# Kernel optimization log

Hardware: AMD Instinct MI355X
Metric: run time of the kernel (lower is better)

## Reference

```python
import jax, jax.numpy as jnp
import numpy as np

N_HEADS = 8

def setup_inputs() -> dict:
    key = jax.random.key(0)
    ks = jax.random.split(key, 5)
    d = 256
    B, N = 2, 4096
    scale = 1.0 / np.sqrt(d)
    return {
        "x_q": jax.random.normal(ks[0], (B, N, d), jnp.float32),
        "x_kv": jax.random.normal(ks[1], (B, N, d), jnp.float32),
        "Wq": jax.random.normal(ks[2], (d, d), jnp.float32) * scale,
        "bq": jnp.zeros((d,), jnp.float32),
        "Wk": jax.random.normal(ks[3], (d, d), jnp.float32) * scale,
        "bk": jnp.zeros((d,), jnp.float32),
        "Wv": jax.random.normal(ks[4], (d, d), jnp.float32) * scale,
        "bv": jnp.zeros((d,), jnp.float32),
    }


def reference(x_q, x_kv, Wq, bq, Wk, bk, Wv, bv):
    B, Nq, d = x_q.shape
    H = N_HEADS
    dh = d // H
    # linear projections (torch Linear: x @ W^T + b)
    q = x_q @ Wq.T + bq            # [B, Nq, d]
    k = x_kv @ Wk.T + bk           # [B, Nk, d]
    v = x_kv @ Wv.T + bv           # [B, Nk, d]
    # split heads -> [B, H, N, dh]
    q = q.reshape(B, Nq, H, dh).transpose(0, 2, 1, 3)
    k = k.reshape(B, -1, H, dh).transpose(0, 2, 1, 3)
    v = v.reshape(B, -1, H, dh).transpose(0, 2, 1, 3)
    # scores [B, H, Nq, Nk], softmax over keys
    scores = jnp.einsum('bhqd,bhkd->bhqk', q, k) / jnp.sqrt(jnp.asarray(dh, q.dtype))
    attn = jax.nn.softmax(scores, axis=-1)
    out = jnp.einsum('bhqk,bhkd->bhqd', attn, v)   # [B, H, Nq, dh]
    return out.transpose(0, 2, 1, 3).reshape(B, Nq, H * dh)
```

## Files before the change

kernel.cpp:

```cpp
#include <hip/hip_runtime.h>
#include <stdint.h>

#define BATCH 2
#define NSEQ 4096
#define DM 256
#define NHEAD 8
#define DH 32
#define SCALE 0.17677669529663687f
#define QPRE (SCALE * 1.44269504088896340736f)

#if __has_builtin(__builtin_amdgcn_exp2f)
#define EXP2W(x) __builtin_amdgcn_exp2f(x)
#else
#define EXP2W(x) exp2f(x)
#endif

typedef unsigned short ushort_t;
typedef __attribute__((ext_vector_type(8))) short short8;
typedef __attribute__((ext_vector_type(4))) float float4v;

__device__ __forceinline__ ushort_t f2bf(float f) {
    union { float f; uint32_t i; } x; x.f = f;
    uint32_t i = x.i;
    i += ((i >> 16) & 1u) + 0x7fffu;
    return (ushort_t)(i >> 16);
}
__device__ __forceinline__ uint32_t rne16(float f) {
    const uint32_t i = __float_as_uint(f);
    return i + 0x7fffu + ((i >> 16) & 1u);
}
#if __has_builtin(__builtin_amdgcn_cvt_pk_bf16_f32)
typedef __bf16 bf16x2_t __attribute__((ext_vector_type(2)));
__device__ __forceinline__ uint32_t pk2(float a, float b) {
    union { bf16x2_t v; uint32_t u; } c;
    c.v = __builtin_amdgcn_cvt_pk_bf16_f32(a, b);
    return c.u;
}
#else
__device__ __forceinline__ uint32_t pk2(float a, float b) {
    return __builtin_amdgcn_perm(rne16(b), rne16(a), 0x07060302u);
}
#endif

__device__ __forceinline__ void load_lds_16B(const void* g, void* lds) {
    __builtin_amdgcn_global_load_lds(
        (const __attribute__((address_space(1))) void*)g,
        (__attribute__((address_space(3))) void*)lds, 16, 0, 0);
}

__global__ __launch_bounds__(256) void packw_kernel(
    const float* __restrict__ Wq, const float* __restrict__ Wk,
    const float* __restrict__ Wv, ushort_t* __restrict__ Wp)
{
    const int mat = blockIdx.x >> 5;
    const int off = (((blockIdx.x & 31) << 8) + threadIdx.x) * 8;
    const float* W = (mat == 0) ? Wq : (mat == 1) ? Wk : Wv;
    const float s  = (mat == 0) ? QPRE : 1.0f;
    float4 a = *(const float4*)(W + off);
    float4 b = *(const float4*)(W + off + 4);
    uint32_t d[4] = { pk2(a.x * s, a.y * s), pk2(a.z * s, a.w * s),
                      pk2(b.x * s, b.y * s), pk2(b.z * s, b.w * s) };
    *(uint4*)(Wp + (size_t)mat * (DM * DM) + off) = *(const uint4*)d;
}

#define RST 264
__global__ __launch_bounds__(256) void proj_kernel(
    const float* __restrict__ x_q, const float* __restrict__ x_kv,
    const ushort_t* __restrict__ Wp,
    const float* __restrict__ bq, const float* __restrict__ bk,
    const float* __restrict__ bv,
    ushort_t* __restrict__ Qh, ushort_t* __restrict__ Kh,
    ushort_t* __restrict__ Vt)
{
    const int mat = blockIdx.y;
    const int n0  = blockIdx.x * 32;
    const float* x    = (mat == 0) ? x_q : x_kv;
    const ushort_t* W = Wp + (size_t)mat * (DM * DM);
    const float* bias = (mat == 0) ? bq : (mat == 1) ? bk : bv;
    const float bscale = (mat == 0) ? QPRE : 1.0f;

    __shared__ __align__(16) ushort_t xls[32 * RST];
    const int t = threadIdx.x;
    {
        const int r  = t >> 3;
        const int c0 = (t & 7) * 32;
        const float* src = x + (size_t)(n0 + r) * DM + c0;
        uint32_t d[16];
        #pragma unroll
        for (int i = 0; i < 8; i++) {
            float4 v = *(const float4*)(src + i * 4);
            d[i * 2]     = pk2(v.x, v.y);
            d[i * 2 + 1] = pk2(v.z, v.w);
        }
        uint32_t* dst = (uint32_t*)&xls[r * RST + c0];
        #pragma unroll
        for (int i = 0; i < 4; i++)
            *(uint4*)(dst + i * 4) = *(const uint4*)&d[i * 4];
    }
    __syncthreads();

    const int w    = t >> 6;
    const int l    = t & 63;
    const int lm   = l & 15;
    const int quad = l >> 4;
    const int j0   = w * 64;

    float4v acc[2][4];
    #pragma unroll
    for (int rt = 0; rt < 2; rt++)
        #pragma unroll
        for (int jt = 0; jt < 4; jt++)
            acc[rt][jt] = (float4v){0.f, 0.f, 0.f, 0.f};

    for (int kc = 0; kc < DM / 32; kc++) {
        short8 af[2];
        #pragma unroll
        for (int rt = 0; rt < 2; rt++)
            af[rt] = *(const short8*)&xls[(rt * 16 + lm) * RST + kc * 32 + quad * 8];
        #pragma unroll
        for (int jt = 0; jt < 4; jt++) {
            short8 bf = *(const short8*)(W + (size_t)(j0 + jt * 16 + lm) * DM
                                           + kc * 32 + quad * 8);
            if (mat == 2) {
                acc[0][jt] = __builtin_amdgcn_mfma_f32_16x16x32_bf16(af[0], bf, acc[0][jt], 0, 0, 0);
                acc[1][jt] = __builtin_amdgcn_mfma_f32_16x16x32_bf16(af[1], bf, acc[1][jt], 0, 0, 0);
            } else {
                acc[0][jt] = __builtin_amdgcn_mfma_f32_16x16x32_bf16(bf, af[0], acc[0][jt], 0, 0, 0);
                acc[1][jt] = __builtin_amdgcn_mfma_f32_16x16x32_bf16(bf, af[1], acc[1][jt], 0, 0, 0);
            }
        }
    }

    const int bb = n0 >> 12;
    const int cn = n0 & (NSEQ - 1);
    if (mat == 2) {
        #pragma unroll
        for (int jt = 0; jt < 4; jt++) {
            const int j  = j0 + jt * 16 + lm;
            const int h  = j >> 5, dd = j & 31;
            const int bh = bb * NHEAD + h;
            const float bj = bias[j];
            #pragma unroll
            for (int rt = 0; rt < 2; rt++) {
                union { ushort_t u[4]; uint2 v; } pk;
                #pragma unroll
                for (int r = 0; r < 4; r++) pk.u[r] = f2bf(acc[rt][jt][r] + bj);
                *(uint2*)&Vt[((size_t)bh * DH + dd) * NSEQ + cn + quad * 8 + rt * 4] = pk.v;
            }
        }
    } else {
        ushort_t* dst = (mat == 0) ? Qh : Kh;
        #pragma unroll
        for (int jt = 0; jt < 4; jt++) {
            const int jb = j0 + jt * 16 + quad * 4;
            const int h  = jb >> 5, dd0 = jb & 31;
            const int bh = bb * NHEAD + h;
            float4 b4 = *(const float4*)(bias + jb);
            #pragma unroll
            for (int rt = 0; rt < 2; rt++) {
                const int n = cn + rt * 16 + lm;
                union { ushort_t u[4]; uint2 v; } pk;
                pk.u[0] = f2bf(acc[rt][jt][0] + b4.x * bscale);
                pk.u[1] = f2bf(acc[rt][jt][1] + b4.y * bscale);
                pk.u[2] = f2bf(acc[rt][jt][2] + b4.z * bscale);
                pk.u[3] = f2bf(acc[rt][jt][3] + b4.w * bscale);
                *(uint2*)&dst[((size_t)bh * NSEQ + n) * DH + dd0] = pk.v;
            }
        }
    }
}

#define QT 2
__global__ __launch_bounds__(256) void fattn_kernel(
    const ushort_t* __restrict__ Qh, const ushort_t* __restrict__ Kh,
    const ushort_t* __restrict__ Vt, float* __restrict__ out)
{
    const int blk  = blockIdx.x;
    const int xcd  = blk & 7;
    const int jj   = blk >> 3;
    const int bh   = xcd * 2 + (jj & 1);
    const int qblk = jj >> 1;
    const int b    = bh >> 3, h = bh & 7;

    const int w    = threadIdx.x >> 6;
    const int l    = threadIdx.x & 63;
    const int lm   = l & 15;
    const int quad = l >> 4;
    const int q0   = qblk * 128 + w * 32;

    __shared__ __align__(16) ushort_t tiles[2][2048];

    const ushort_t* Qb = Qh + (size_t)bh * NSEQ * DH;
    const ushort_t* Kb = Kh + (size_t)bh * NSEQ * DH;
    const ushort_t* Vb = Vt + (size_t)bh * DH * NSEQ;

    const ushort_t* gsrc;
    int gadv;
    if (w < 2) { gsrc = Kb + (size_t)(w * 16 + (l >> 2)) * DH + (l & 3) * 8;  gadv = 32 * DH; }
    else       { gsrc = Vb + (size_t)((w - 2) * 16 + (l >> 2)) * NSEQ + (l & 3) * 8; gadv = 32; }

    short8 qf[QT];
    #pragma unroll
    for (int qt = 0; qt < QT; qt++)
        qf[qt] = *(const short8*)(Qb + (size_t)(q0 + qt * 16 + lm) * DH + quad * 8);

    short8 ones;
    #pragma unroll
    for (int i = 0; i < 8; i++) ones[i] = (short)0x3F80;

    float4v accO[QT][2], accL[QT];
    #pragma unroll
    for (int qt = 0; qt < QT; qt++) {
        accO[qt][0] = (float4v){0.f, 0.f, 0.f, 0.f};
        accO[qt][1] = (float4v){0.f, 0.f, 0.f, 0.f};
        accL[qt]    = (float4v){0.f, 0.f, 0.f, 0.f};
    }
    const float4v zero = {0.f, 0.f, 0.f, 0.f};

    load_lds_16B(gsrc, &tiles[0][w * 512]);
    gsrc += gadv;

    for (int it = 0; it < NSEQ / 32; it++) {
        __syncthreads();
        if (it < NSEQ / 32 - 1) {
            load_lds_16B(gsrc, &tiles[(it + 1) & 1][w * 512]);
            gsrc += gadv;
        }

        const ushort_t* Kt = &tiles[it & 1][0];
        const ushort_t* Vl = &tiles[it & 1][1024];
        short8 kf0 = *(const short8*)&Kt[lm * 32 + quad * 8];
        short8 kf1 = *(const short8*)&Kt[512 + lm * 32 + quad * 8];
        short8 vf0 = *(const short8*)&Vl[lm * 32 + quad * 8];
        short8 vf1 = *(const short8*)&Vl[512 + lm * 32 + quad * 8];

        #pragma unroll
        for (int qt = 0; qt < QT; qt++) {
            float4v s0 = __builtin_amdgcn_mfma_f32_16x16x32_bf16(kf0, qf[qt], zero, 0, 0, 0);
            float4v s1 = __builtin_amdgcn_mfma_f32_16x16x32_bf16(kf1, qf[qt], zero, 0, 0, 0);
            float p0[4], p1[4];
            #pragma unroll
            for (int r = 0; r < 4; r++) {
                p0[r] = EXP2W(s0[r]);
                p1[r] = EXP2W(s1[r]);
            }
            uint32_t pd[4] = { pk2(p0[0], p0[1]), pk2(p0[2], p0[3]),
                               pk2(p1[0], p1[1]), pk2(p1[2], p1[3]) };
            short8 pf = *(const short8*)pd;
            accO[qt][0] = __builtin_amdgcn_mfma_f32_16x16x32_bf16(pf, vf0, accO[qt][0], 0, 0, 0);
            accO[qt][1] = __builtin_amdgcn_mfma_f32_16x16x32_bf16(pf, vf1, accO[qt][1], 0, 0, 0);
            accL[qt]    = __builtin_amdgcn_mfma_f32_16x16x32_bf16(pf, ones, accL[qt], 0, 0, 0);
        }
    }

    #pragma unroll
    for (int qt = 0; qt < QT; qt++)
        #pragma unroll
        for (int r = 0; r < 4; r++) {
            const float inv = 1.0f / accL[qt][r];
            const int q = q0 + qt * 16 + quad * 4 + r;
            float* orow = out + ((size_t)b * NSEQ + q) * DM + h * DH;
            orow[lm]      = accO[qt][0][r] * inv;
            orow[16 + lm] = accO[qt][1][r] * inv;
        }
}

extern "C" void kernel_launch(void* const* d_in, const int* in_sizes, int n_in,
                              void* d_out, int out_size, void* d_ws, size_t ws_size,
                              hipStream_t stream)
{
    const float* x_q  = (const float*)d_in[0];
    const float* x_kv = (const float*)d_in[1];
    const float* Wq   = (const float*)d_in[2];
    const float* bq   = (const float*)d_in[3];
    const float* Wk   = (const float*)d_in[4];
    const float* bk   = (const float*)d_in[5];
    const float* Wv   = (const float*)d_in[6];
    const float* bv   = (const float*)d_in[7];
    float* out = (float*)d_out;

    const size_t per = (size_t)BATCH * NHEAD * NSEQ * DH;
    ushort_t* Qh = (ushort_t*)d_ws;
    ushort_t* Kh = Qh + per;
    ushort_t* Vt = Kh + per;
    ushort_t* Wp = (ushort_t*)d_out;

    packw_kernel<<<96, 256, 0, stream>>>(Wq, Wk, Wv, Wp);

    dim3 pgrid(BATCH * NSEQ / 32, 3);
    proj_kernel<<<pgrid, 256, 0, stream>>>(x_q, x_kv, Wp, bq, bk, bv,
                                           Qh, Kh, Vt);

    fattn_kernel<<<512, 256, 0, stream>>>(Qh, Kh, Vt, out);
}
```

Measured before the change: 168.4 us.

## Split attention over key halves with a combine kernel for more blocks

Adds a split-K flash attention kernel: each of 1024 blocks handles half the keys and writes an unnormalized partial output and row sum, and a combine kernel adds the two halves and normalizes. This doubles the block count, so the 256 CUs of the GPU are better occupied than with 512 blocks. The cost is an extra launch and an extra read and write pass over the output-sized buffers. It also adds an explicit vmcnt(0) wait before the barrier in the tile loop of both kernels. That makes the async LDS loads visible, but it may serialize the prefetch.

Measured after the change: 168.5 us. No clear change (+0.0%).

```diff
diff --git a/kernel.cpp b/kernel.cpp
--- a/kernel.cpp
+++ b/kernel.cpp
@@ -14,6 +14,8 @@
 #else
 #define EXP2W(x) exp2f(x)
 #endif
+
+#define WAIT_VM0() asm volatile("s_waitcnt vmcnt(0)" ::: "memory")
 
 typedef unsigned short ushort_t;
 typedef __attribute__((ext_vector_type(8))) short short8;
@@ -221,6 +223,7 @@
     gsrc += gadv;
 
     for (int it = 0; it < NSEQ / 32; it++) {
+        WAIT_VM0();
         __syncthreads();
         if (it < NSEQ / 32 - 1) {
             load_lds_16B(gsrc, &tiles[(it + 1) & 1][w * 512]);
@@ -265,6 +268,133 @@
         }
 }
 
+#define KITERS 64
+__global__ __launch_bounds__(256) void fattn_split_kernel(
+    const ushort_t* __restrict__ Qh, const ushort_t* __restrict__ Kh,
+    const ushort_t* __restrict__ Vt, float* __restrict__ out,
+    float* __restrict__ Opart, float* __restrict__ Lp)
+{
+    const int blk  = blockIdx.x;
+    const int xcd  = blk & 7;
+    const int jj   = blk >> 3;
+    const int bh   = xcd * 2 + (jj & 1);
+    const int qblk = (jj >> 1) & 31;
+    const int khalf = jj >> 6;
+    const int b    = bh >> 3, h = bh & 7;
+
+    const int w    = threadIdx.x >> 6;
+    const int l    = threadIdx.x & 63;
+    const int lm   = l & 15;
+    const int quad = l >> 4;
+    const int q0   = qblk * 128 + w * 32;
+
+    __shared__ __align__(16) ushort_t tiles[2][2048];
+
+    const ushort_t* Qb = Qh + (size_t)bh * NSEQ * DH;
+    const ushort_t* Kb = Kh + (size_t)bh * NSEQ * DH + (size_t)khalf * 2048 * DH;
+    const ushort_t* Vb = Vt + (size_t)bh * DH * NSEQ + (size_t)khalf * 2048;
+
+    const ushort_t* gsrc;
+    int gadv;
+    if (w < 2) { gsrc = Kb + (size_t)(w * 16 + (l >> 2)) * DH + (l & 3) * 8;  gadv = 32 * DH; }
+    else       { gsrc = Vb + (size_t)((w - 2) * 16 + (l >> 2)) * NSEQ + (l & 3) * 8; gadv = 32; }
+
+    short8 qf[QT];
+    #pragma unroll
+    for (int qt = 0; qt < QT; qt++)
+        qf[qt] = *(const short8*)(Qb + (size_t)(q0 + qt * 16 + lm) * DH + quad * 8);
+
+    short8 ones;
+    #pragma unroll
+    for (int i = 0; i < 8; i++) ones[i] = (short)0x3F80;
+
+    float4v accO[QT][2], accL[QT];
+    #pragma unroll
+    for (int qt = 0; qt < QT; qt++) {
+        accO[qt][0] = (float4v){0.f, 0.f, 0.f, 0.f};
+        accO[qt][1] = (float4v){0.f, 0.f, 0.f, 0.f};
+        accL[qt]    = (float4v){0.f, 0.f, 0.f, 0.f};
+    }
+    const float4v zero = {0.f, 0.f, 0.f, 0.f};
+
+    load_lds_16B(gsrc, &tiles[0][w * 512]);
+    gsrc += gadv;
+
+    for (int it = 0; it < KITERS; it++) {
+        WAIT_VM0();
+        __syncthreads();
+        if (it < KITERS - 1) {
+            load_lds_16B(gsrc, &tiles[(it + 1) & 1][w * 512]);
+            gsrc += gadv;
+        }
+
+        const ushort_t* Kt = &tiles[it & 1][0];
+        const ushort_t* Vl = &tiles[it & 1][1024];
+        short8 kf0 = *(const short8*)&Kt[lm * 32 + quad * 8];
+        short8 kf1 = *(const short8*)&Kt[512 + lm * 32 + quad * 8];
+        short8 vf0 = *(const short8*)&Vl[lm * 32 + quad * 8];
+        short8 vf1 = *(const short8*)&Vl[512 + lm * 32 + quad * 8];
+
+        #pragma unroll
+        for (int qt = 0; qt < QT; qt++) {
+            float4v s0 = __builtin_amdgcn_mfma_f32_16x16x32_bf16(kf0, qf[qt], zero, 0, 0, 0);
+            float4v s1 = __builtin_amdgcn_mfma_f32_16x16x32_bf16(kf1, qf[qt], zero, 0, 0, 0);
+            float p0[4], p1[4];
+            #pragma unroll
+            for (int r = 0; r < 4; r++) {
+                p0[r] = EXP2W(s0[r]);
+                p1[r] = EXP2W(s1[r]);
+            }
+            uint32_t pd[4] = { pk2(p0[0], p0[1]), pk2(p0[2], p0[3]),
+                               pk2(p1[0], p1[1]), pk2(p1[2], p1[3]) };
+            short8 pf = *(const short8*)pd;
+            accO[qt][0] = __builtin_amdgcn_mfma_f32_16x16x32_bf16(pf, vf0, accO[qt][0], 0, 0, 0);
+            accO[qt][1] = __builtin_amdgcn_mfma_f32_16x16x32_bf16(pf, vf1, accO[qt][1], 0, 0, 0);
+            accL[qt]    = __builtin_amdgcn_mfma_f32_16x16x32_bf16(pf, ones, accL[qt], 0, 0, 0);
+        }
+    }
+
+    float* Od = (khalf == 0) ? out : Opart;
+    #pragma unroll
+    for (int qt = 0; qt < QT; qt++)
+        #pragma unroll
+        for (int r = 0; r < 4; r++) {
+            const int q = q0 + qt * 16 + quad * 4 + r;
+            float* orow = Od + ((size_t)b * NSEQ + q) * DM + h * DH;
+            orow[lm]      = accO[qt][0][r];
+            orow[16 + lm] = accO[qt][1][r];
+            if (lm == 0)
+                Lp[khalf * (16 * NSEQ) + bh * NSEQ + q] = accL[qt][r];
+        }
+}
+
+__global__ __launch_bounds__(256) void combine_kernel(
+    float* __restrict__ out, const float* __restrict__ Opart,
+    const float* __restrict__ Lp)
+{
+    const int t   = blockIdx.x * 256 + threadIdx.x;
+    const size_t base = (size_t)t * 8;
+    const int b   = (int)(base >> 20);
+    const int rem = (int)(base & ((1u << 20) - 1));
+    const int q   = rem >> 8;
+    const int dm  = rem & 255;
+    const int h   = dm >> 5;
+    const int bh  = b * NHEAD + h;
+    const float l0 = Lp[bh * NSEQ + q];
+    const float l1 = Lp[16 * NSEQ + bh * NSEQ + q];
+    const float inv = 1.0f / (l0 + l1);
+    float4 a0 = *(const float4*)(out + base);
+    float4 a1 = *(const float4*)(out + base + 4);
+    float4 c0 = *(const float4*)(Opart + base);
+    float4 c1 = *(const float4*)(Opart + base + 4);
+    a0.x = (a0.x + c0.x) * inv;  a0.y = (a0.y + c0.y) * inv;
+    a0.z = (a0.z + c0.z) * inv;  a0.w = (a0.w + c0.w) * inv;
+    a1.x = (a1.x + c1.x) * inv;  a1.y = (a1.y + c1.y) * inv;
+    a1.z = (a1.z + c1.z) * inv;  a1.w = (a1.w + c1.w) * inv;
+    *(float4*)(out + base)     = a0;
+    *(float4*)(out + base + 4) = a1;
+}
+
 extern "C" void kernel_launch(void* const* d_in, const int* in_sizes, int n_in,
                               void* d_out, int out_size, void* d_ws, size_t ws_size,
                               hipStream_t stream)
@@ -285,11 +415,23 @@
     ushort_t* Vt = Kh + per;
     ushort_t* Wp = (ushort_t*)d_out;
 
+    const size_t qkv_bytes   = per * 3 * sizeof(ushort_t);
+    const size_t opart_elems = (size_t)BATCH * NSEQ * DM;
+    const size_t lp_elems    = (size_t)2 * 16 * NSEQ;
+    const size_t need = qkv_bytes + (opart_elems + lp_elems) * sizeof(float);
+    float* Opart = (float*)((char*)d_ws + qkv_bytes);
+    float* Lp    = Opart + opart_elems;
+
     packw_kernel<<<96, 256, 0, stream>>>(Wq, Wk, Wv, Wp);
 
     dim3 pgrid(BATCH * NSEQ / 32, 3);
     proj_kernel<<<pgrid, 256, 0, stream>>>(x_q, x_kv, Wp, bq, bk, bv,
                                            Qh, Kh, Vt);
 
-    fattn_kernel<<<512, 256, 0, stream>>>(Qh, Kh, Vt, out);
-}
+    if (ws_size >= need) {
+        fattn_split_kernel<<<1024, 256, 0, stream>>>(Qh, Kh, Vt, out, Opart, Lp);
+        combine_kernel<<<(BATCH * NSEQ * DM) / (256 * 8), 256, 0, stream>>>(out, Opart, Lp);
+    } else {
+        fattn_kernel<<<512, 256, 0, stream>>>(Qh, Kh, Vt, out);
+    }
+}
```
